# Kernel optimization log

Measured on AMD Instinct MI355X. Metric: run time of the kernel, lower is better.

Reference implementation:

```python
import jax, jax.numpy as jnp
import numpy as np

N_BLOCKS = 8
HIDDEN = 256
BATCH = 4096
IN_DIM = 3 * N_BLOCKS


def setup_inputs() -> dict:
    key = jax.random.key(0)
    ks = jax.random.split(key, 32)
    s = 0.05
    d = {}
    d['x'] = jax.random.normal(ks[0], (BATCH, IN_DIM), dtype=jnp.float32)
    # per-block object encoders (stacked): in -> H, relu, H -> H, relu, H -> H
    d['o_W0'] = jax.random.normal(ks[1], (N_BLOCKS, IN_DIM, HIDDEN), dtype=jnp.float32) * s
    d['o_b0'] = jnp.zeros((N_BLOCKS, HIDDEN), jnp.float32)
    d['o_W1'] = jax.random.normal(ks[2], (N_BLOCKS, HIDDEN, HIDDEN), dtype=jnp.float32) * s
    d['o_b1'] = jnp.zeros((N_BLOCKS, HIDDEN), jnp.float32)
    d['o_W2'] = jax.random.normal(ks[3], (N_BLOCKS, HIDDEN, HIDDEN), dtype=jnp.float32) * s
    d['o_b2'] = jnp.zeros((N_BLOCKS, HIDDEN), jnp.float32)
    # clear predicate encoder: H -> H, relu, H -> H, relu, H -> 1, sigmoid
    d['c_W0'] = jax.random.normal(ks[4], (HIDDEN, HIDDEN), dtype=jnp.float32) * s
    d['c_b0'] = jnp.zeros((HIDDEN,), jnp.float32)
    d['c_W1'] = jax.random.normal(ks[5], (HIDDEN, HIDDEN), dtype=jnp.float32) * s
    d['c_b1'] = jnp.zeros((HIDDEN,), jnp.float32)
    d['c_W2'] = jax.random.normal(ks[6], (HIDDEN, 1), dtype=jnp.float32) * s
    d['c_b2'] = jnp.zeros((1,), jnp.float32)
    # ontable predicate encoder
    d['t_W0'] = jax.random.normal(ks[7], (HIDDEN, HIDDEN), dtype=jnp.float32) * s
    d['t_b0'] = jnp.zeros((HIDDEN,), jnp.float32)
    d['t_W1'] = jax.random.normal(ks[8], (HIDDEN, HIDDEN), dtype=jnp.float32) * s
    d['t_b1'] = jnp.zeros((HIDDEN,), jnp.float32)
    d['t_W2'] = jax.random.normal(ks[9], (HIDDEN, 1), dtype=jnp.float32) * s
    d['t_b2'] = jnp.zeros((1,), jnp.float32)
    # AonB predicate encoder: 2H -> H, relu, H -> H, relu, H -> 1, sigmoid
    d['a_W0'] = jax.random.normal(ks[10], (2 * HIDDEN, HIDDEN), dtype=jnp.float32) * s
    d['a_b0'] = jnp.zeros((HIDDEN,), jnp.float32)
    d['a_W1'] = jax.random.normal(ks[11], (HIDDEN, HIDDEN), dtype=jnp.float32) * s
    d['a_b1'] = jnp.zeros((HIDDEN,), jnp.float32)
    d['a_W2'] = jax.random.normal(ks[12], (HIDDEN, 1), dtype=jnp.float32) * s
    d['a_b2'] = jnp.zeros((1,), jnp.float32)
    return d


def _pred_mlp(h, W0, b0, W1, b1, W2, b2):
    h = jax.nn.relu(h @ W0 + b0)
    h = jax.nn.relu(h @ W1 + b1)
    return jax.nn.sigmoid(h @ W2 + b2)


def reference(x, o_W0, o_b0, o_W1, o_b1, o_W2, o_b2,
              c_W0, c_b0, c_W1, c_b1, c_W2, c_b2,
              t_W0, t_b0, t_W1, t_b1, t_W2, t_b2,
              a_W0, a_b0, a_W1, a_b1, a_W2, a_b2):
    B = x.shape[0]
    H = o_W0.shape[-1]
    # object encodings: (N, B, H), all N encoders batched via einsum
    h = jax.nn.relu(jnp.einsum('bd,ndh->nbh', x, o_W0) + o_b0[:, None, :])
    h = jax.nn.relu(jnp.einsum('nbh,nhk->nbk', h, o_W1) + o_b1[:, None, :])
    enc = jnp.einsum('nbh,nhk->nbk', h, o_W2) + o_b2[:, None, :]
    # clear/ontable predicates: (N, B, 1) -> (B, N)
    clear = _pred_mlp(enc, c_W0, c_b0, c_W1, c_b1, c_W2, c_b2)[..., 0].T
    table = _pred_mlp(enc, t_W0, t_b0, t_W1, t_b1, t_W2, t_b2)[..., 0].T
    # AonB over all pairs; split first layer to avoid materializing (N,N,B,2H)
    a_l = jnp.einsum('nbh,hk->nbk', enc, a_W0[:H])
    a_r = jnp.einsum('nbh,hk->nbk', enc, a_W0[H:])
    ph = jax.nn.relu(a_l[:, None] + a_r[None, :] + a_b0)  # (N, N, B, H), axis0=i(left), axis1=j(right)
    ph = jax.nn.relu(ph @ a_W1 + a_b1)
    aonb = jax.nn.sigmoid(ph @ a_W2 + a_b2)[..., 0]  # (N, N, B)
    aonb_b = jnp.transpose(aonb, (2, 0, 1))  # (B, N, N)
    # per block i: [AonB(i,0..N-1), clear(i), ontable(i)] concatenated over i
    out = jnp.concatenate([aonb_b, clear[..., None], table[..., None]], axis=2)
    return out.reshape(B, -1)
```

## Files before the change

### kernel.cpp

```cpp
#include <hip/hip_runtime.h>
#include <hip/hip_bf16.h>

#define OFF_O0   0u
#define OFF_O1   65536u
#define OFF_O2   589824u
#define OFF_C0   1114112u
#define OFF_C1   1179648u
#define OFF_T0   1245184u
#define OFF_T1   1310720u
#define OFF_AL   1376256u
#define OFF_AR   1441792u
#define OFF_A1   1507328u
#define OFF_ENC  1572864u
#define OFF_ALQ  9961472u
#define OFF_ARQ  18350080u

typedef short s8v __attribute__((ext_vector_type(8)));
typedef float f4v __attribute__((ext_vector_type(4)));

__device__ __forceinline__ unsigned short f2bf(float f) {
  unsigned u = __float_as_uint(f);
  unsigned r = (u + 0x7FFFu + ((u >> 16) & 1u)) >> 16;
  return (unsigned short)r;
}
__device__ __forceinline__ float bf2f(unsigned short h) {
  return __uint_as_float(((unsigned)h) << 16);
}

__device__ __forceinline__ void gemm_epilogue(
    f4v acc[4][4], const float* bias, int act,
    unsigned short* outb, unsigned short* gout)
{
  int lane = threadIdx.x & 63;
  int w    = threadIdx.x >> 6;
  int lr = lane & 15, kh = lane >> 4;
  if (outb) __syncthreads();
  #pragma unroll
  for (int nt = 0; nt < 4; nt++) {
    int col = w*64 + nt*16 + lr;
    float bv = bias ? bias[col] : 0.0f;
    #pragma unroll
    for (int mt = 0; mt < 4; mt++) {
      #pragma unroll
      for (int i = 0; i < 4; i++) {
        int row = mt*16 + kh*4 + i;
        float v = acc[mt][nt][i] + bv;
        if (act) v = fmaxf(v, 0.0f);
        unsigned short hh = f2bf(v);
        if (outb) {
          int bofs = (2*col) ^ ((row & 7) << 4);
          *(unsigned short*)((char*)outb + row*512 + bofs) = hh;
        }
        if (gout) gout[row*256 + col] = hh;
      }
    }
  }
  if (outb) __syncthreads();
}

__device__ __forceinline__ void gemm_core(
    const unsigned short* inb, const unsigned short* __restrict__ wt,
    f4v acc[4][4])
{
  int lane = threadIdx.x & 63;
  int w    = threadIdx.x >> 6;
  int lr = lane & 15, kh = lane >> 4;
  #pragma unroll
  for (int a = 0; a < 4; a++)
    #pragma unroll
    for (int b = 0; b < 4; b++) acc[a][b] = (f4v){0.f,0.f,0.f,0.f};

  #pragma unroll
  for (int k0 = 0; k0 < 256; k0 += 32) {
    s8v bfrag[4];
    #pragma unroll
    for (int nt = 0; nt < 4; nt++)
      bfrag[nt] = *(const s8v*)(wt + (w*64 + nt*16 + lr)*256 + k0 + kh*8);
    #pragma unroll
    for (int mt = 0; mt < 4; mt++) {
      int row = mt*16 + lr;
      int bofs = (2*k0 + kh*16) ^ ((row & 7) << 4);
      s8v afrag = *(const s8v*)((const char*)inb + row*512 + bofs);
      #pragma unroll
      for (int nt = 0; nt < 4; nt++)
        acc[mt][nt] = __builtin_amdgcn_mfma_f32_16x16x32_bf16(afrag, bfrag[nt], acc[mt][nt], 0, 0, 0);
    }
  }
}

__device__ __forceinline__ void gemm64(
    const unsigned short* inb, const unsigned short* __restrict__ wt,
    const float* bias, int act, unsigned short* outb, unsigned short* gout)
{
  f4v acc[4][4];
  gemm_core(inb, wt, acc);
  gemm_epilogue(acc, bias, act, outb, gout);
}

__device__ __forceinline__ void gemm64_dot(
    const unsigned short* inb, const unsigned short* __restrict__ wt,
    const float* __restrict__ bias, const float* __restrict__ w2, float b2,
    float* __restrict__ out, int m0, int offs, float* red)
{
  int lane = threadIdx.x & 63;
  int w    = threadIdx.x >> 6;
  int lr = lane & 15, kh = lane >> 4;
  f4v acc[4][4];
  gemm_core(inb, wt, acc);

  float w2v[4], bv[4];
  #pragma unroll
  for (int nt = 0; nt < 4; nt++) {
    int col = w*64 + nt*16 + lr;
    w2v[nt] = w2[col];
    bv[nt]  = bias[col];
  }
  #pragma unroll
  for (int mt = 0; mt < 4; mt++) {
    #pragma unroll
    for (int i = 0; i < 4; i++) {
      float s = 0.0f;
      #pragma unroll
      for (int nt = 0; nt < 4; nt++)
        s += fmaxf(acc[mt][nt][i] + bv[nt], 0.0f) * w2v[nt];
      s += __shfl_xor(s, 1);
      s += __shfl_xor(s, 2);
      s += __shfl_xor(s, 4);
      s += __shfl_xor(s, 8);
      if (lr == 0) red[w*64 + mt*16 + kh*4 + i] = s;
    }
  }
  __syncthreads();
  if (threadIdx.x < 64) {
    int row = threadIdx.x;
    float s = red[row] + red[64 + row] + red[128 + row] + red[192 + row];
    out[(m0 + row)*80 + offs] = 1.0f / (1.0f + __expf(-s - b2));
  }
}

__device__ __forceinline__ void gemm_x(
    const unsigned short* xb, const unsigned short* __restrict__ wt,
    const float* bias, unsigned short* outb)
{
  int lane = threadIdx.x & 63;
  int w    = threadIdx.x >> 6;
  int lr = lane & 15, kh = lane >> 4;
  f4v acc[4][4];
  #pragma unroll
  for (int a = 0; a < 4; a++)
    #pragma unroll
    for (int b = 0; b < 4; b++) acc[a][b] = (f4v){0.f,0.f,0.f,0.f};

  s8v bfrag[4];
  #pragma unroll
  for (int nt = 0; nt < 4; nt++)
    bfrag[nt] = *(const s8v*)(wt + (w*64 + nt*16 + lr)*32 + kh*8);
  #pragma unroll
  for (int mt = 0; mt < 4; mt++) {
    s8v afrag = *(const s8v*)(xb + (mt*16 + lr)*32 + kh*8);
    #pragma unroll
    for (int nt = 0; nt < 4; nt++)
      acc[mt][nt] = __builtin_amdgcn_mfma_f32_16x16x32_bf16(afrag, bfrag[nt], acc[mt][nt], 0, 0, 0);
  }
  gemm_epilogue(acc, bias, 1, outb, nullptr);
}

__global__ __launch_bounds__(256) void prep_kernel(
    const float* __restrict__ oW0, const float* __restrict__ oW1,
    const float* __restrict__ oW2, const float* __restrict__ cW0,
    const float* __restrict__ cW1, const float* __restrict__ tW0,
    const float* __restrict__ tW1, const float* __restrict__ aW0,
    const float* __restrict__ aW1, unsigned short* __restrict__ ws)
{
  __shared__ float t[32][33];
  int b = blockIdx.x;
  if (b < 1472) {
    int m = b >> 6, tile = b & 63;
    const float* src; unsigned short* dst;
    if      (m < 8)  { src = oW1 + m*65536;       dst = ws + OFF_O1 + m*65536; }
    else if (m < 16) { src = oW2 + (m-8)*65536;   dst = ws + OFF_O2 + (m-8)*65536; }
    else if (m == 16){ src = cW0;                 dst = ws + OFF_C0; }
    else if (m == 17){ src = cW1;                 dst = ws + OFF_C1; }
    else if (m == 18){ src = tW0;                 dst = ws + OFF_T0; }
    else if (m == 19){ src = tW1;                 dst = ws + OFF_T1; }
    else if (m == 20){ src = aW1;                 dst = ws + OFF_A1; }
    else if (m == 21){ src = aW0;                 dst = ws + OFF_AL; }
    else             { src = aW0 + 65536;         dst = ws + OFF_AR; }
    int kt = tile & 7, nt = tile >> 3;
    int tx = threadIdx.x & 31, ty = threadIdx.x >> 5;
    #pragma unroll
    for (int r = 0; r < 4; r++) {
      int ky = ty*4 + r;
      t[ky][tx] = src[(kt*32 + ky)*256 + nt*32 + tx];
    }
    __syncthreads();
    #pragma unroll
    for (int r = 0; r < 4; r++) {
      int ny = ty*4 + r;
      dst[(nt*32 + ny)*256 + kt*32 + tx] = f2bf(t[tx][ny]);
    }
  } else {
    int idx = (b - 1472)*256 + threadIdx.x;
    int k = idx & 31, n2 = (idx >> 5) & 255, nb = idx >> 13;
    float v = (k < 24) ? oW0[(nb*24 + k)*256 + n2] : 0.0f;
    ws[OFF_O0 + idx] = f2bf(v);
  }
}

__global__ __launch_bounds__(256) void encoder_kernel(
    const float* __restrict__ x,
    const float* __restrict__ ob0, const float* __restrict__ ob1,
    const float* __restrict__ ob2, const float* __restrict__ ab0,
    unsigned short* __restrict__ ws)
{
  __shared__ unsigned short buf[64*256];
  __shared__ unsigned short xb[64*32];
  int n  = blockIdx.x >> 6;
  int m0 = (blockIdx.x & 63) * 64;

  for (int t = threadIdx.x; t < 64*32; t += 256) {
    int row = t >> 5, c = t & 31;
    xb[t] = f2bf(c < 24 ? x[(m0 + row)*24 + c] : 0.0f);
  }
  __syncthreads();
  gemm_x (xb,  ws + OFF_O0 + n*8192,  ob0 + n*256, buf);
  gemm64 (buf, ws + OFF_O1 + n*65536, ob1 + n*256, 1, buf, nullptr);
  gemm64 (buf, ws + OFF_O2 + n*65536, ob2 + n*256, 0, buf,
          ws + OFF_ENC + (unsigned)(n*4096 + m0)*256);
  gemm64 (buf, ws + OFF_AL, nullptr, 0, nullptr,
          ws + OFF_ALQ + (unsigned)(n*4096 + m0)*256);
  gemm64 (buf, ws + OFF_AR, ab0, 0, nullptr,
          ws + OFF_ARQ + (unsigned)(n*4096 + m0)*256);
}

__global__ __launch_bounds__(256) void tail_kernel(
    const unsigned short* __restrict__ ws,
    const float* __restrict__ ab1, const float* __restrict__ aW2,
    const float* __restrict__ ab2,
    const float* __restrict__ cb0, const float* __restrict__ cb1,
    const float* __restrict__ cW2, const float* __restrict__ cb2,
    const float* __restrict__ tb0, const float* __restrict__ tb1,
    const float* __restrict__ tW2, const float* __restrict__ tb2,
    float* __restrict__ out)
{
  __shared__ unsigned short bufA[64*256];
  __shared__ float red[256];
  int b = blockIdx.x;
  if (b < 4096) {
    int m0   = (b & 63) * 64;
    int pair = b >> 6;
    int i = pair >> 3, j = pair & 7;
    const unsigned short* Lp = ws + OFF_ALQ + (unsigned)(i*4096 + m0)*256;
    const unsigned short* Rp = ws + OFF_ARQ + (unsigned)(j*4096 + m0)*256;
    for (int t = threadIdx.x; t < 64*32; t += 256) {
      int row = t >> 5, chunk = t & 31;
      s8v l8 = *(const s8v*)(Lp + row*256 + chunk*8);
      s8v r8 = *(const s8v*)(Rp + row*256 + chunk*8);
      s8v o8;
      #pragma unroll
      for (int e = 0; e < 8; e++) {
        float v = bf2f((unsigned short)l8[e]) + bf2f((unsigned short)r8[e]);
        o8[e] = (short)f2bf(fmaxf(v, 0.0f));
      }
      int bofs = (chunk*16) ^ ((row & 7) << 4);
      *(s8v*)((char*)bufA + row*512 + bofs) = o8;
    }
    __syncthreads();
    gemm64_dot(bufA, ws + OFF_A1, ab1, aW2, ab2[0], out, m0, i*10 + j, red);
  } else {
    int b2 = b - 4096;
    int p  = b2 >> 9;
    int n  = (b2 >> 6) & 7;
    int m0 = (b2 & 63) * 64;
    const unsigned short* encp = ws + OFF_ENC + (unsigned)(n*4096 + m0)*256;
    for (int t = threadIdx.x; t < 64*32; t += 256) {
      int row = t >> 5, chunk = t & 31;
      s8v v = *(const s8v*)(encp + row*256 + chunk*8);
      int bofs = (chunk*16) ^ ((row & 7) << 4);
      *(s8v*)((char*)bufA + row*512 + bofs) = v;
    }
    __syncthreads();
    const unsigned short* W0 = ws + (p ? OFF_T0 : OFF_C0);
    const unsigned short* W1 = ws + (p ? OFF_T1 : OFF_C1);
    gemm64(bufA, W0, p ? tb0 : cb0, 1, bufA, nullptr);
    gemm64_dot(bufA, W1, p ? tb1 : cb1, p ? tW2 : cW2,
               p ? tb2[0] : cb2[0], out, m0, n*10 + 8 + p, red);
  }
}

extern "C" void kernel_launch(void* const* d_in, const int* in_sizes, int n_in,
                              void* d_out, int out_size, void* d_ws, size_t ws_size,
                              hipStream_t stream) {
  (void)in_sizes; (void)n_in; (void)out_size; (void)ws_size;
  const float* x   = (const float*)d_in[0];
  const float* oW0 = (const float*)d_in[1];
  const float* ob0 = (const float*)d_in[2];
  const float* oW1 = (const float*)d_in[3];
  const float* ob1 = (const float*)d_in[4];
  const float* oW2 = (const float*)d_in[5];
  const float* ob2 = (const float*)d_in[6];
  const float* cW0 = (const float*)d_in[7];
  const float* cb0 = (const float*)d_in[8];
  const float* cW1 = (const float*)d_in[9];
  const float* cb1 = (const float*)d_in[10];
  const float* cW2 = (const float*)d_in[11];
  const float* cb2 = (const float*)d_in[12];
  const float* tW0 = (const float*)d_in[13];
  const float* tb0 = (const float*)d_in[14];
  const float* tW1 = (const float*)d_in[15];
  const float* tb1 = (const float*)d_in[16];
  const float* tW2 = (const float*)d_in[17];
  const float* tb2 = (const float*)d_in[18];
  const float* aW0 = (const float*)d_in[19];
  const float* ab0 = (const float*)d_in[20];
  const float* aW1 = (const float*)d_in[21];
  const float* ab1 = (const float*)d_in[22];
  const float* aW2 = (const float*)d_in[23];
  const float* ab2 = (const float*)d_in[24];
  unsigned short* ws = (unsigned short*)d_ws;
  float* out = (float*)d_out;

  hipLaunchKernelGGL(prep_kernel, dim3(1728), dim3(256), 0, stream,
                     oW0, oW1, oW2, cW0, cW1, tW0, tW1, aW0, aW1, ws);
  hipLaunchKernelGGL(encoder_kernel, dim3(512), dim3(256), 0, stream,
                     x, ob0, ob1, ob2, ab0, ws);
  hipLaunchKernelGGL(tail_kernel, dim3(5120), dim3(256), 0, stream,
                     ws, ab1, aW2, ab2, cb0, cb1, cW2, cb2,
                     tb0, tb1, tW2, tb2, out);
}
```

Measured before the change: 185.8 us.

## Restructure AonB tail: one block per left object, loop over right objects with double buffering

```diff
diff --git a/kernel.cpp b/kernel.cpp
--- a/kernel.cpp
+++ b/kernel.cpp
@@ -233,7 +233,7 @@
           ws + OFF_ARQ + (unsigned)(n*4096 + m0)*256);
 }
 
-__global__ __launch_bounds__(256) void tail_kernel(
+__global__ __launch_bounds__(256, 4) void tail_kernel(
     const unsigned short* __restrict__ ws,
     const float* __restrict__ ab1, const float* __restrict__ aW2,
     const float* __restrict__ ab2,
@@ -246,32 +246,121 @@
   __shared__ unsigned short bufA[64*256];
   __shared__ float red[256];
   int b = blockIdx.x;
-  if (b < 4096) {
-    int m0   = (b & 63) * 64;
-    int pair = b >> 6;
-    int i = pair >> 3, j = pair & 7;
-    const unsigned short* Lp = ws + OFF_ALQ + (unsigned)(i*4096 + m0)*256;
-    const unsigned short* Rp = ws + OFF_ARQ + (unsigned)(j*4096 + m0)*256;
-    for (int t = threadIdx.x; t < 64*32; t += 256) {
-      int row = t >> 5, chunk = t & 31;
-      s8v l8 = *(const s8v*)(Lp + row*256 + chunk*8);
-      s8v r8 = *(const s8v*)(Rp + row*256 + chunk*8);
+  int lane = threadIdx.x & 63;
+  int w    = threadIdx.x >> 6;
+  int lr = lane & 15, kh = lane >> 4;
+
+  if (b < 1024) {
+    int i  = b >> 7;
+    int m0 = (b & 127) * 32;
+    const unsigned short* Lp    = ws + OFF_ALQ + (unsigned)(i*4096 + m0)*256;
+    const unsigned short* Rbase = ws + OFF_ARQ + (unsigned)m0*256;
+    const unsigned short* wt    = ws + OFF_A1;
+
+    int t5   = threadIdx.x >> 5;
+    int colc = threadIdx.x & 31;
+    unsigned goff[4]; int lofs[4];
+    s8v L[4];
+    #pragma unroll
+    for (int q = 0; q < 4; q++) {
+      int row = q*8 + t5;
+      goff[q] = (unsigned)row*256 + colc*8;
+      lofs[q] = row*512 + ((colc*16) ^ (t5 << 4));
+      L[q] = *(const s8v*)(Lp + goff[q]);
+    }
+    float w2v[4], bv[4];
+    #pragma unroll
+    for (int nt = 0; nt < 4; nt++) {
+      int col = w*64 + nt*16 + lr;
+      w2v[nt] = aW2[col];
+      bv[nt]  = ab1[col];
+    }
+    float b2 = ab2[0];
+
+    #pragma unroll
+    for (int q = 0; q < 4; q++) {
+      s8v r8 = *(const s8v*)(Rbase + goff[q]);
       s8v o8;
       #pragma unroll
       for (int e = 0; e < 8; e++) {
-        float v = bf2f((unsigned short)l8[e]) + bf2f((unsigned short)r8[e]);
+        float v = bf2f((unsigned short)L[q][e]) + bf2f((unsigned short)r8[e]);
         o8[e] = (short)f2bf(fmaxf(v, 0.0f));
       }
-      int bofs = (chunk*16) ^ ((row & 7) << 4);
-      *(s8v*)((char*)bufA + row*512 + bofs) = o8;
+      *(s8v*)((char*)bufA + lofs[q]) = o8;
     }
     __syncthreads();
-    gemm64_dot(bufA, ws + OFF_A1, ab1, aW2, ab2[0], out, m0, i*10 + j, red);
+
+    for (int j = 0; j < 8; j++) {
+      int cur = j & 1;
+      const unsigned short* inb = bufA + cur*(32*256);
+      s8v Rr[4];
+      if (j < 7) {
+        const unsigned short* Rp = Rbase + (unsigned)(j+1)*(4096u*256u);
+        #pragma unroll
+        for (int q = 0; q < 4; q++) Rr[q] = *(const s8v*)(Rp + goff[q]);
+      }
+      f4v acc[2][4];
+      #pragma unroll
+      for (int a = 0; a < 2; a++)
+        #pragma unroll
+        for (int c = 0; c < 4; c++) acc[a][c] = (f4v){0.f,0.f,0.f,0.f};
+      #pragma unroll
+      for (int k0 = 0; k0 < 256; k0 += 32) {
+        s8v bfrag[4];
+        #pragma unroll
+        for (int nt = 0; nt < 4; nt++)
+          bfrag[nt] = *(const s8v*)(wt + (w*64 + nt*16 + lr)*256 + k0 + kh*8);
+        #pragma unroll
+        for (int mt = 0; mt < 2; mt++) {
+          int row = mt*16 + lr;
+          int bofs = (2*k0 + kh*16) ^ ((row & 7) << 4);
+          s8v afrag = *(const s8v*)((const char*)inb + row*512 + bofs);
+          #pragma unroll
+          for (int nt = 0; nt < 4; nt++)
+            acc[mt][nt] = __builtin_amdgcn_mfma_f32_16x16x32_bf16(afrag, bfrag[nt], acc[mt][nt], 0, 0, 0);
+        }
+      }
+      if (j < 7) {
+        char* ob = (char*)(bufA + (cur ^ 1)*(32*256));
+        #pragma unroll
+        for (int q = 0; q < 4; q++) {
+          s8v o8;
+          #pragma unroll
+          for (int e = 0; e < 8; e++) {
+            float v = bf2f((unsigned short)L[q][e]) + bf2f((unsigned short)Rr[q][e]);
+            o8[e] = (short)f2bf(fmaxf(v, 0.0f));
+          }
+          *(s8v*)(ob + lofs[q]) = o8;
+        }
+      }
+      #pragma unroll
+      for (int mt = 0; mt < 2; mt++) {
+        #pragma unroll
+        for (int ii = 0; ii < 4; ii++) {
+          float s = 0.0f;
+          #pragma unroll
+          for (int nt = 0; nt < 4; nt++)
+            s += fmaxf(acc[mt][nt][ii] + bv[nt], 0.0f) * w2v[nt];
+          s += __shfl_xor(s, 1);
+          s += __shfl_xor(s, 2);
+          s += __shfl_xor(s, 4);
+          s += __shfl_xor(s, 8);
+          if (lr == 0) red[cur*128 + w*32 + mt*16 + kh*4 + ii] = s;
+        }
+      }
+      __syncthreads();
+      if (threadIdx.x < 32) {
+        int row = threadIdx.x;
+        float s = red[cur*128 + row] + red[cur*128 + 32 + row]
+                + red[cur*128 + 64 + row] + red[cur*128 + 96 + row];
+        out[(m0 + row)*80 + i*10 + j] = 1.0f / (1.0f + __expf(-s - b2));
+      }
+    }
   } else {
-    int b2 = b - 4096;
-    int p  = b2 >> 9;
-    int n  = (b2 >> 6) & 7;
-    int m0 = (b2 & 63) * 64;
+    int b2i = b - 1024;
+    int p   = b2i >> 9;
+    int n   = (b2i >> 6) & 7;
+    int m0  = (b2i & 63) * 64;
     const unsigned short* encp = ws + OFF_ENC + (unsigned)(n*4096 + m0)*256;
     for (int t = threadIdx.x; t < 64*32; t += 256) {
       int row = t >> 5, chunk = t & 31;
@@ -324,7 +413,7 @@
                      oW0, oW1, oW2, cW0, cW1, tW0, tW1, aW0, aW1, ws);
   hipLaunchKernelGGL(encoder_kernel, dim3(512), dim3(256), 0, stream,
                      x, ob0, ob1, ob2, ab0, ws);
-  hipLaunchKernelGGL(tail_kernel, dim3(5120), dim3(256), 0, stream,
+  hipLaunchKernelGGL(tail_kernel, dim3(2048), dim3(256), 0, stream,
                      ws, ab1, aW2, ab2, cb0, cb1, cW2, cb2,
                      tb0, tb1, tW2, tb2, out);
 }
```

Result: slower. 284.1 us (+52.9%).

## Grow GEMM row tile to 128 with 8-wave blocks in encoder and tail

Applied to the files above, without the earlier changes.

```diff
diff --git a/kernel.cpp b/kernel.cpp
--- a/kernel.cpp
+++ b/kernel.cpp
@@ -27,23 +27,56 @@
   return __uint_as_float(((unsigned)h) << 16);
 }
 
-__device__ __forceinline__ void gemm_epilogue(
+
+__device__ __forceinline__ void gemm_core128(
+    const unsigned short* inb, const unsigned short* __restrict__ wt,
+    f4v acc[4][4])
+{
+  int lane = threadIdx.x & 63;
+  int w    = threadIdx.x >> 6;
+  int wm = w >> 2, wn = w & 3;
+  int lr = lane & 15, kh = lane >> 4;
+  #pragma unroll
+  for (int a = 0; a < 4; a++)
+    #pragma unroll
+    for (int b = 0; b < 4; b++) acc[a][b] = (f4v){0.f,0.f,0.f,0.f};
+
+  #pragma unroll
+  for (int k0 = 0; k0 < 256; k0 += 32) {
+    s8v bfrag[4];
+    #pragma unroll
+    for (int nt = 0; nt < 4; nt++)
+      bfrag[nt] = *(const s8v*)(wt + (wn*64 + nt*16 + lr)*256 + k0 + kh*8);
+    #pragma unroll
+    for (int mt = 0; mt < 4; mt++) {
+      int row = wm*64 + mt*16 + lr;
+      int bofs = (2*k0 + kh*16) ^ ((row & 7) << 4);
+      s8v afrag = *(const s8v*)((const char*)inb + row*512 + bofs);
+      #pragma unroll
+      for (int nt = 0; nt < 4; nt++)
+        acc[mt][nt] = __builtin_amdgcn_mfma_f32_16x16x32_bf16(afrag, bfrag[nt], acc[mt][nt], 0, 0, 0);
+    }
+  }
+}
+
+__device__ __forceinline__ void gemm_epi128(
     f4v acc[4][4], const float* bias, int act,
     unsigned short* outb, unsigned short* gout)
 {
   int lane = threadIdx.x & 63;
   int w    = threadIdx.x >> 6;
+  int wm = w >> 2, wn = w & 3;
   int lr = lane & 15, kh = lane >> 4;
   if (outb) __syncthreads();
   #pragma unroll
   for (int nt = 0; nt < 4; nt++) {
-    int col = w*64 + nt*16 + lr;
+    int col = wn*64 + nt*16 + lr;
     float bv = bias ? bias[col] : 0.0f;
     #pragma unroll
     for (int mt = 0; mt < 4; mt++) {
       #pragma unroll
       for (int i = 0; i < 4; i++) {
-        int row = mt*16 + kh*4 + i;
+        int row = wm*64 + mt*16 + kh*4 + i;
         float v = acc[mt][nt][i] + bv;
         if (act) v = fmaxf(v, 0.0f);
         unsigned short hh = f2bf(v);
@@ -58,60 +91,31 @@
   if (outb) __syncthreads();
 }
 
-__device__ __forceinline__ void gemm_core(
-    const unsigned short* inb, const unsigned short* __restrict__ wt,
-    f4v acc[4][4])
-{
-  int lane = threadIdx.x & 63;
-  int w    = threadIdx.x >> 6;
-  int lr = lane & 15, kh = lane >> 4;
-  #pragma unroll
-  for (int a = 0; a < 4; a++)
-    #pragma unroll
-    for (int b = 0; b < 4; b++) acc[a][b] = (f4v){0.f,0.f,0.f,0.f};
-
-  #pragma unroll
-  for (int k0 = 0; k0 < 256; k0 += 32) {
-    s8v bfrag[4];
-    #pragma unroll
-    for (int nt = 0; nt < 4; nt++)
-      bfrag[nt] = *(const s8v*)(wt + (w*64 + nt*16 + lr)*256 + k0 + kh*8);
-    #pragma unroll
-    for (int mt = 0; mt < 4; mt++) {
-      int row = mt*16 + lr;
-      int bofs = (2*k0 + kh*16) ^ ((row & 7) << 4);
-      s8v afrag = *(const s8v*)((const char*)inb + row*512 + bofs);
-      #pragma unroll
-      for (int nt = 0; nt < 4; nt++)
-        acc[mt][nt] = __builtin_amdgcn_mfma_f32_16x16x32_bf16(afrag, bfrag[nt], acc[mt][nt], 0, 0, 0);
-    }
-  }
-}
-
-__device__ __forceinline__ void gemm64(
+__device__ __forceinline__ void gemm128(
     const unsigned short* inb, const unsigned short* __restrict__ wt,
     const float* bias, int act, unsigned short* outb, unsigned short* gout)
 {
   f4v acc[4][4];
-  gemm_core(inb, wt, acc);
-  gemm_epilogue(acc, bias, act, outb, gout);
-}
-
-__device__ __forceinline__ void gemm64_dot(
+  gemm_core128(inb, wt, acc);
+  gemm_epi128(acc, bias, act, outb, gout);
+}
+
+__device__ __forceinline__ void gemm128_dot(
     const unsigned short* inb, const unsigned short* __restrict__ wt,
     const float* __restrict__ bias, const float* __restrict__ w2, float b2,
     float* __restrict__ out, int m0, int offs, float* red)
 {
   int lane = threadIdx.x & 63;
   int w    = threadIdx.x >> 6;
+  int wm = w >> 2, wn = w & 3;
   int lr = lane & 15, kh = lane >> 4;
   f4v acc[4][4];
-  gemm_core(inb, wt, acc);
+  gemm_core128(inb, wt, acc);
 
   float w2v[4], bv[4];
   #pragma unroll
   for (int nt = 0; nt < 4; nt++) {
-    int col = w*64 + nt*16 + lr;
+    int col = wn*64 + nt*16 + lr;
     w2v[nt] = w2[col];
     bv[nt]  = bias[col];
   }
@@ -127,23 +131,24 @@
       s += __shfl_xor(s, 2);
       s += __shfl_xor(s, 4);
       s += __shfl_xor(s, 8);
-      if (lr == 0) red[w*64 + mt*16 + kh*4 + i] = s;
+      if (lr == 0) red[(wm*64 + mt*16 + kh*4 + i)*4 + wn] = s;
     }
   }
   __syncthreads();
-  if (threadIdx.x < 64) {
+  if (threadIdx.x < 128) {
     int row = threadIdx.x;
-    float s = red[row] + red[64 + row] + red[128 + row] + red[192 + row];
+    float s = red[row*4] + red[row*4+1] + red[row*4+2] + red[row*4+3];
     out[(m0 + row)*80 + offs] = 1.0f / (1.0f + __expf(-s - b2));
   }
 }
 
-__device__ __forceinline__ void gemm_x(
+__device__ __forceinline__ void gemm_x128(
     const unsigned short* xb, const unsigned short* __restrict__ wt,
     const float* bias, unsigned short* outb)
 {
   int lane = threadIdx.x & 63;
   int w    = threadIdx.x >> 6;
+  int wm = w >> 2, wn = w & 3;
   int lr = lane & 15, kh = lane >> 4;
   f4v acc[4][4];
   #pragma unroll
@@ -154,15 +159,15 @@
   s8v bfrag[4];
   #pragma unroll
   for (int nt = 0; nt < 4; nt++)
-    bfrag[nt] = *(const s8v*)(wt + (w*64 + nt*16 + lr)*32 + kh*8);
+    bfrag[nt] = *(const s8v*)(wt + (wn*64 + nt*16 + lr)*32 + kh*8);
   #pragma unroll
   for (int mt = 0; mt < 4; mt++) {
-    s8v afrag = *(const s8v*)(xb + (mt*16 + lr)*32 + kh*8);
+    s8v afrag = *(const s8v*)(xb + (wm*64 + mt*16 + lr)*32 + kh*8);
     #pragma unroll
     for (int nt = 0; nt < 4; nt++)
       acc[mt][nt] = __builtin_amdgcn_mfma_f32_16x16x32_bf16(afrag, bfrag[nt], acc[mt][nt], 0, 0, 0);
   }
-  gemm_epilogue(acc, bias, 1, outb, nullptr);
+  gemm_epi128(acc, bias, 1, outb, nullptr);
 }
 
 __global__ __launch_bounds__(256) void prep_kernel(
@@ -207,33 +212,40 @@
   }
 }
 
-__global__ __launch_bounds__(256) void encoder_kernel(
+__global__ __launch_bounds__(512) void encoder_kernel(
     const float* __restrict__ x,
     const float* __restrict__ ob0, const float* __restrict__ ob1,
     const float* __restrict__ ob2, const float* __restrict__ ab0,
     unsigned short* __restrict__ ws)
 {
-  __shared__ unsigned short buf[64*256];
-  __shared__ unsigned short xb[64*32];
-  int n  = blockIdx.x >> 6;
-  int m0 = (blockIdx.x & 63) * 64;
-
-  for (int t = threadIdx.x; t < 64*32; t += 256) {
-    int row = t >> 5, c = t & 31;
-    xb[t] = f2bf(c < 24 ? x[(m0 + row)*24 + c] : 0.0f);
+  __shared__ unsigned short buf[128*256];
+  __shared__ unsigned short xb[128*32];
+  int n  = blockIdx.x >> 5;
+  int m0 = (blockIdx.x & 31) * 128;
+
+  {
+    int t = threadIdx.x;
+    int row = t >> 2, chunk = t & 3;
+    s8v o8;
+    #pragma unroll
+    for (int e = 0; e < 8; e++) {
+      int c = chunk*8 + e;
+      o8[e] = (short)f2bf(c < 24 ? x[(m0 + row)*24 + c] : 0.0f);
+    }
+    *(s8v*)(xb + row*32 + chunk*8) = o8;
   }
   __syncthreads();
-  gemm_x (xb,  ws + OFF_O0 + n*8192,  ob0 + n*256, buf);
-  gemm64 (buf, ws + OFF_O1 + n*65536, ob1 + n*256, 1, buf, nullptr);
-  gemm64 (buf, ws + OFF_O2 + n*65536, ob2 + n*256, 0, buf,
-          ws + OFF_ENC + (unsigned)(n*4096 + m0)*256);
-  gemm64 (buf, ws + OFF_AL, nullptr, 0, nullptr,
-          ws + OFF_ALQ + (unsigned)(n*4096 + m0)*256);
-  gemm64 (buf, ws + OFF_AR, ab0, 0, nullptr,
-          ws + OFF_ARQ + (unsigned)(n*4096 + m0)*256);
-}
-
-__global__ __launch_bounds__(256) void tail_kernel(
+  gemm_x128(xb,  ws + OFF_O0 + n*8192,  ob0 + n*256, buf);
+  gemm128 (buf, ws + OFF_O1 + n*65536, ob1 + n*256, 1, buf, nullptr);
+  gemm128 (buf, ws + OFF_O2 + n*65536, ob2 + n*256, 0, buf,
+           ws + OFF_ENC + (unsigned)(n*4096 + m0)*256);
+  gemm128 (buf, ws + OFF_AL, nullptr, 0, nullptr,
+           ws + OFF_ALQ + (unsigned)(n*4096 + m0)*256);
+  gemm128 (buf, ws + OFF_AR, ab0, 0, nullptr,
+           ws + OFF_ARQ + (unsigned)(n*4096 + m0)*256);
+}
+
+__global__ __launch_bounds__(512) void tail_kernel(
     const unsigned short* __restrict__ ws,
     const float* __restrict__ ab1, const float* __restrict__ aW2,
     const float* __restrict__ ab2,
@@ -243,17 +255,20 @@
     const float* __restrict__ tW2, const float* __restrict__ tb2,
     float* __restrict__ out)
 {
-  __shared__ unsigned short bufA[64*256];
-  __shared__ float red[256];
+  __shared__ unsigned short bufA[128*256];
+  __shared__ float red[512];
   int b = blockIdx.x;
-  if (b < 4096) {
-    int m0   = (b & 63) * 64;
-    int pair = b >> 6;
-    int i = pair >> 3, j = pair & 7;
+
+  if (b < 2048) {
+    int i  = b >> 8;
+    int j  = (b >> 5) & 7;
+    int m0 = (b & 31) * 128;
     const unsigned short* Lp = ws + OFF_ALQ + (unsigned)(i*4096 + m0)*256;
     const unsigned short* Rp = ws + OFF_ARQ + (unsigned)(j*4096 + m0)*256;
-    for (int t = threadIdx.x; t < 64*32; t += 256) {
-      int row = t >> 5, chunk = t & 31;
+    #pragma unroll
+    for (int q = 0; q < 8; q++) {
+      int idx = q*512 + threadIdx.x;
+      int row = idx >> 5, chunk = idx & 31;
       s8v l8 = *(const s8v*)(Lp + row*256 + chunk*8);
       s8v r8 = *(const s8v*)(Rp + row*256 + chunk*8);
       s8v o8;
@@ -266,15 +281,17 @@
       *(s8v*)((char*)bufA + row*512 + bofs) = o8;
     }
     __syncthreads();
-    gemm64_dot(bufA, ws + OFF_A1, ab1, aW2, ab2[0], out, m0, i*10 + j, red);
+    gemm128_dot(bufA, ws + OFF_A1, ab1, aW2, ab2[0], out, m0, i*10 + j, red);
   } else {
-    int b2 = b - 4096;
-    int p  = b2 >> 9;
-    int n  = (b2 >> 6) & 7;
-    int m0 = (b2 & 63) * 64;
+    int b2i = b - 2048;
+    int p   = b2i >> 8;
+    int n   = (b2i >> 5) & 7;
+    int m0  = (b2i & 31) * 128;
     const unsigned short* encp = ws + OFF_ENC + (unsigned)(n*4096 + m0)*256;
-    for (int t = threadIdx.x; t < 64*32; t += 256) {
-      int row = t >> 5, chunk = t & 31;
+    #pragma unroll
+    for (int q = 0; q < 8; q++) {
+      int idx = q*512 + threadIdx.x;
+      int row = idx >> 5, chunk = idx & 31;
       s8v v = *(const s8v*)(encp + row*256 + chunk*8);
       int bofs = (chunk*16) ^ ((row & 7) << 4);
       *(s8v*)((char*)bufA + row*512 + bofs) = v;
@@ -282,9 +299,9 @@
     __syncthreads();
     const unsigned short* W0 = ws + (p ? OFF_T0 : OFF_C0);
     const unsigned short* W1 = ws + (p ? OFF_T1 : OFF_C1);
-    gemm64(bufA, W0, p ? tb0 : cb0, 1, bufA, nullptr);
-    gemm64_dot(bufA, W1, p ? tb1 : cb1, p ? tW2 : cW2,
-               p ? tb2[0] : cb2[0], out, m0, n*10 + 8 + p, red);
+    gemm128(bufA, W0, p ? tb0 : cb0, 1, bufA, nullptr);
+    gemm128_dot(bufA, W1, p ? tb1 : cb1, p ? tW2 : cW2,
+                p ? tb2[0] : cb2[0], out, m0, n*10 + 8 + p, red);
   }
 }
 
@@ -322,9 +339,9 @@
 
   hipLaunchKernelGGL(prep_kernel, dim3(1728), dim3(256), 0, stream,
                      oW0, oW1, oW2, cW0, cW1, tW0, tW1, aW0, aW1, ws);
-  hipLaunchKernelGGL(encoder_kernel, dim3(512), dim3(256), 0, stream,
+  hipLaunchKernelGGL(encoder_kernel, dim3(256), dim3(512), 0, stream,
                      x, ob0, ob1, ob2, ab0, ws);
-  hipLaunchKernelGGL(tail_kernel, dim3(5120), dim3(256), 0, stream,
+  hipLaunchKernelGGL(tail_kernel, dim3(2560), dim3(512), 0, stream,
                      ws, ab1, aW2, ab2, cb0, cb1, cW2, cb2,
                      tb0, tb1, tW2, tb2, out);
 }
```

Result: slower. 207.3 us (+11.5%).

## Split tail into pair and predicate kernels with direct global A-fragment loads

Applied to the files above, without the earlier changes.

```diff
diff --git a/kernel.cpp b/kernel.cpp
--- a/kernel.cpp
+++ b/kernel.cpp
@@ -27,6 +27,7 @@
   return __uint_as_float(((unsigned)h) << 16);
 }
 
+
 __device__ __forceinline__ void gemm_epilogue(
     f4v acc[4][4], const float* bias, int act,
     unsigned short* outb, unsigned short* gout)
@@ -69,7 +70,6 @@
   for (int a = 0; a < 4; a++)
     #pragma unroll
     for (int b = 0; b < 4; b++) acc[a][b] = (f4v){0.f,0.f,0.f,0.f};
-
   #pragma unroll
   for (int k0 = 0; k0 < 256; k0 += 32) {
     s8v bfrag[4];
@@ -88,6 +88,34 @@
   }
 }
 
+__device__ __forceinline__ void gemm_core_gA(
+    const unsigned short* __restrict__ ga,
+    const unsigned short* __restrict__ wt,
+    f4v acc[4][4])
+{
+  int lane = threadIdx.x & 63;
+  int w    = threadIdx.x >> 6;
+  int lr = lane & 15, kh = lane >> 4;
+  #pragma unroll
+  for (int a = 0; a < 4; a++)
+    #pragma unroll
+    for (int b = 0; b < 4; b++) acc[a][b] = (f4v){0.f,0.f,0.f,0.f};
+  #pragma unroll
+  for (int k0 = 0; k0 < 256; k0 += 32) {
+    s8v bfrag[4];
+    #pragma unroll
+    for (int nt = 0; nt < 4; nt++)
+      bfrag[nt] = *(const s8v*)(wt + (w*64 + nt*16 + lr)*256 + k0 + kh*8);
+    #pragma unroll
+    for (int mt = 0; mt < 4; mt++) {
+      s8v afrag = *(const s8v*)(ga + (mt*16 + lr)*256 + k0 + kh*8);
+      #pragma unroll
+      for (int nt = 0; nt < 4; nt++)
+        acc[mt][nt] = __builtin_amdgcn_mfma_f32_16x16x32_bf16(afrag, bfrag[nt], acc[mt][nt], 0, 0, 0);
+    }
+  }
+}
+
 __device__ __forceinline__ void gemm64(
     const unsigned short* inb, const unsigned short* __restrict__ wt,
     const float* bias, int act, unsigned short* outb, unsigned short* gout)
@@ -97,17 +125,14 @@
   gemm_epilogue(acc, bias, act, outb, gout);
 }
 
-__device__ __forceinline__ void gemm64_dot(
-    const unsigned short* inb, const unsigned short* __restrict__ wt,
-    const float* __restrict__ bias, const float* __restrict__ w2, float b2,
+__device__ __forceinline__ void dot_tail(
+    f4v acc[4][4], const float* __restrict__ bias,
+    const float* __restrict__ w2, float b2,
     float* __restrict__ out, int m0, int offs, float* red)
 {
   int lane = threadIdx.x & 63;
   int w    = threadIdx.x >> 6;
   int lr = lane & 15, kh = lane >> 4;
-  f4v acc[4][4];
-  gemm_core(inb, wt, acc);
-
   float w2v[4], bv[4];
   #pragma unroll
   for (int nt = 0; nt < 4; nt++) {
@@ -127,20 +152,21 @@
       s += __shfl_xor(s, 2);
       s += __shfl_xor(s, 4);
       s += __shfl_xor(s, 8);
-      if (lr == 0) red[w*64 + mt*16 + kh*4 + i] = s;
+      if (lr == 0) red[(mt*16 + kh*4 + i)*4 + w] = s;
     }
   }
   __syncthreads();
   if (threadIdx.x < 64) {
     int row = threadIdx.x;
-    float s = red[row] + red[64 + row] + red[128 + row] + red[192 + row];
+    float s = red[row*4] + red[row*4+1] + red[row*4+2] + red[row*4+3];
     out[(m0 + row)*80 + offs] = 1.0f / (1.0f + __expf(-s - b2));
   }
 }
 
-__device__ __forceinline__ void gemm_x(
-    const unsigned short* xb, const unsigned short* __restrict__ wt,
-    const float* bias, unsigned short* outb)
+__device__ __forceinline__ void gemm_xg(
+    const float* __restrict__ xg, int m0,
+    const unsigned short* __restrict__ wt, const float* bias,
+    unsigned short* outb)
 {
   int lane = threadIdx.x & 63;
   int w    = threadIdx.x >> 6;
@@ -157,10 +183,15 @@
     bfrag[nt] = *(const s8v*)(wt + (w*64 + nt*16 + lr)*32 + kh*8);
   #pragma unroll
   for (int mt = 0; mt < 4; mt++) {
-    s8v afrag = *(const s8v*)(xb + (mt*16 + lr)*32 + kh*8);
+    s8v a8 = (s8v){0,0,0,0,0,0,0,0};
+    if (kh < 3) {
+      const float* px = xg + (m0 + mt*16 + lr)*24 + kh*8;
+      #pragma unroll
+      for (int e = 0; e < 8; e++) a8[e] = (short)f2bf(px[e]);
+    }
     #pragma unroll
     for (int nt = 0; nt < 4; nt++)
-      acc[mt][nt] = __builtin_amdgcn_mfma_f32_16x16x32_bf16(afrag, bfrag[nt], acc[mt][nt], 0, 0, 0);
+      acc[mt][nt] = __builtin_amdgcn_mfma_f32_16x16x32_bf16(a8, bfrag[nt], acc[mt][nt], 0, 0, 0);
   }
   gemm_epilogue(acc, bias, 1, outb, nullptr);
 }
@@ -214,16 +245,12 @@
     unsigned short* __restrict__ ws)
 {
   __shared__ unsigned short buf[64*256];
-  __shared__ unsigned short xb[64*32];
-  int n  = blockIdx.x >> 6;
-  int m0 = (blockIdx.x & 63) * 64;
-
-  for (int t = threadIdx.x; t < 64*32; t += 256) {
-    int row = t >> 5, c = t & 31;
-    xb[t] = f2bf(c < 24 ? x[(m0 + row)*24 + c] : 0.0f);
-  }
-  __syncthreads();
-  gemm_x (xb,  ws + OFF_O0 + n*8192,  ob0 + n*256, buf);
+  int b = blockIdx.x;
+  int wsw = (b & 7)*64 + (b >> 3);
+  int n  = wsw >> 6;
+  int m0 = (wsw & 63) * 64;
+
+  gemm_xg(x, m0, ws + OFF_O0 + n*8192, ob0 + n*256, buf);
   gemm64 (buf, ws + OFF_O1 + n*65536, ob1 + n*256, 1, buf, nullptr);
   gemm64 (buf, ws + OFF_O2 + n*65536, ob2 + n*256, 0, buf,
           ws + OFF_ENC + (unsigned)(n*4096 + m0)*256);
@@ -233,59 +260,79 @@
           ws + OFF_ARQ + (unsigned)(n*4096 + m0)*256);
 }
 
-__global__ __launch_bounds__(256) void tail_kernel(
+__global__ __launch_bounds__(256) void pair_kernel(
     const unsigned short* __restrict__ ws,
     const float* __restrict__ ab1, const float* __restrict__ aW2,
-    const float* __restrict__ ab2,
+    const float* __restrict__ ab2, float* __restrict__ out)
+{
+  __shared__ float red[256];
+  int b = blockIdx.x;
+  int wsw = (b & 7)*512 + (b >> 3);
+  int chunk = wsw >> 6, pair = wsw & 63;
+  int i = pair >> 3, j = pair & 7;
+  int m0 = chunk * 64;
+  const unsigned short* Lp = ws + OFF_ALQ + (unsigned)(i*4096 + m0)*256;
+  const unsigned short* Rp = ws + OFF_ARQ + (unsigned)(j*4096 + m0)*256;
+  const unsigned short* wt = ws + OFF_A1;
+
+  int lane = threadIdx.x & 63;
+  int w    = threadIdx.x >> 6;
+  int lr = lane & 15, kh = lane >> 4;
+
+  f4v acc[4][4];
+  #pragma unroll
+  for (int a = 0; a < 4; a++)
+    #pragma unroll
+    for (int c = 0; c < 4; c++) acc[a][c] = (f4v){0.f,0.f,0.f,0.f};
+
+  #pragma unroll
+  for (int k0 = 0; k0 < 256; k0 += 32) {
+    s8v bfrag[4];
+    #pragma unroll
+    for (int nt = 0; nt < 4; nt++)
+      bfrag[nt] = *(const s8v*)(wt + (w*64 + nt*16 + lr)*256 + k0 + kh*8);
+    #pragma unroll
+    for (int mt = 0; mt < 4; mt++) {
+      int ro = (mt*16 + lr)*256 + k0 + kh*8;
+      s8v l8 = *(const s8v*)(Lp + ro);
+      s8v r8 = *(const s8v*)(Rp + ro);
+      s8v a8;
+      #pragma unroll
+      for (int e = 0; e < 8; e++) {
+        float v = bf2f((unsigned short)l8[e]) + bf2f((unsigned short)r8[e]);
+        a8[e] = (short)f2bf(fmaxf(v, 0.0f));
+      }
+      #pragma unroll
+      for (int nt = 0; nt < 4; nt++)
+        acc[mt][nt] = __builtin_amdgcn_mfma_f32_16x16x32_bf16(a8, bfrag[nt], acc[mt][nt], 0, 0, 0);
+    }
+  }
+  dot_tail(acc, ab1, aW2, ab2[0], out, m0, i*10 + j, red);
+}
+
+__global__ __launch_bounds__(256) void pred_kernel(
+    const unsigned short* __restrict__ ws,
     const float* __restrict__ cb0, const float* __restrict__ cb1,
     const float* __restrict__ cW2, const float* __restrict__ cb2,
     const float* __restrict__ tb0, const float* __restrict__ tb1,
     const float* __restrict__ tW2, const float* __restrict__ tb2,
     float* __restrict__ out)
 {
-  __shared__ unsigned short bufA[64*256];
+  __shared__ unsigned short h1[64*256];
   __shared__ float red[256];
   int b = blockIdx.x;
-  if (b < 4096) {
-    int m0   = (b & 63) * 64;
-    int pair = b >> 6;
-    int i = pair >> 3, j = pair & 7;
-    const unsigned short* Lp = ws + OFF_ALQ + (unsigned)(i*4096 + m0)*256;
-    const unsigned short* Rp = ws + OFF_ARQ + (unsigned)(j*4096 + m0)*256;
-    for (int t = threadIdx.x; t < 64*32; t += 256) {
-      int row = t >> 5, chunk = t & 31;
-      s8v l8 = *(const s8v*)(Lp + row*256 + chunk*8);
-      s8v r8 = *(const s8v*)(Rp + row*256 + chunk*8);
-      s8v o8;
-      #pragma unroll
-      for (int e = 0; e < 8; e++) {
-        float v = bf2f((unsigned short)l8[e]) + bf2f((unsigned short)r8[e]);
-        o8[e] = (short)f2bf(fmaxf(v, 0.0f));
-      }
-      int bofs = (chunk*16) ^ ((row & 7) << 4);
-      *(s8v*)((char*)bufA + row*512 + bofs) = o8;
-    }
-    __syncthreads();
-    gemm64_dot(bufA, ws + OFF_A1, ab1, aW2, ab2[0], out, m0, i*10 + j, red);
-  } else {
-    int b2 = b - 4096;
-    int p  = b2 >> 9;
-    int n  = (b2 >> 6) & 7;
-    int m0 = (b2 & 63) * 64;
-    const unsigned short* encp = ws + OFF_ENC + (unsigned)(n*4096 + m0)*256;
-    for (int t = threadIdx.x; t < 64*32; t += 256) {
-      int row = t >> 5, chunk = t & 31;
-      s8v v = *(const s8v*)(encp + row*256 + chunk*8);
-      int bofs = (chunk*16) ^ ((row & 7) << 4);
-      *(s8v*)((char*)bufA + row*512 + bofs) = v;
-    }
-    __syncthreads();
-    const unsigned short* W0 = ws + (p ? OFF_T0 : OFF_C0);
-    const unsigned short* W1 = ws + (p ? OFF_T1 : OFF_C1);
-    gemm64(bufA, W0, p ? tb0 : cb0, 1, bufA, nullptr);
-    gemm64_dot(bufA, W1, p ? tb1 : cb1, p ? tW2 : cW2,
-               p ? tb2[0] : cb2[0], out, m0, n*10 + 8 + p, red);
-  }
+  int wsw = (b & 7)*128 + (b >> 3);
+  int p   = wsw >> 9;
+  int n   = (wsw >> 6) & 7;
+  int m0  = (wsw & 63) * 64;
+  const unsigned short* encp = ws + OFF_ENC + (unsigned)(n*4096 + m0)*256;
+
+  f4v acc[4][4];
+  gemm_core_gA(encp, ws + (p ? OFF_T0 : OFF_C0), acc);
+  gemm_epilogue(acc, p ? tb0 : cb0, 1, h1, nullptr);
+  gemm_core(h1, ws + (p ? OFF_T1 : OFF_C1), acc);
+  dot_tail(acc, p ? tb1 : cb1, p ? tW2 : cW2, p ? tb2[0] : cb2[0],
+           out, m0, n*10 + 8 + p, red);
 }
 
 extern "C" void kernel_launch(void* const* d_in, const int* in_sizes, int n_in,
@@ -324,7 +371,8 @@
                      oW0, oW1, oW2, cW0, cW1, tW0, tW1, aW0, aW1, ws);
   hipLaunchKernelGGL(encoder_kernel, dim3(512), dim3(256), 0, stream,
                      x, ob0, ob1, ob2, ab0, ws);
-  hipLaunchKernelGGL(tail_kernel, dim3(5120), dim3(256), 0, stream,
-                     ws, ab1, aW2, ab2, cb0, cb1, cW2, cb2,
-                     tb0, tb1, tW2, tb2, out);
-}
+  hipLaunchKernelGGL(pair_kernel, dim3(4096), dim3(256), 0, stream,
+                     ws, ab1, aW2, ab2, out);
+  hipLaunchKernelGGL(pred_kernel, dim3(1024), dim3(256), 0, stream,
+                     ws, cb0, cb1, cW2, cb2, tb0, tb1, tW2, tb2, out);
+}
```

Measured after the change: 329.4 us. 1.77x slower.
